# Kernel tuning notes

Measured on AMD Instinct MI355X. Metric: run time of the kernel, lower is better.

The kernel has to match this reference:

```python
import jax, jax.numpy as jnp
import numpy as np

TOP_K = 2

def setup_inputs() -> dict:
    key = jax.random.key(0)
    k1, k2 = jax.random.split(key)
    x = jax.random.normal(k1, (8, 4096, 4096), dtype=jnp.float32)
    # nn.Linear weight [num_experts, dim]
    gate_w = jax.random.normal(k2, (64, 4096), dtype=jnp.float32) * (1.0 / np.sqrt(4096))
    return {"x": x, "gate_w": gate_w}

def reference(x, gate_w):
    # logits: [B, S, E]
    logits = jnp.einsum('bsd,ed->bse', x, gate_w)
    routing_weights = jax.nn.softmax(logits, axis=-1)
    top_weights, top_indices = jax.lax.top_k(routing_weights, TOP_K)
    top_weights = top_weights / jnp.sum(top_weights, axis=-1, keepdims=True)
    return top_weights, top_indices
```

## Files before the change

### kernel.cpp

```cpp
#include <hip/hip_runtime.h>
#include <hip/hip_bf16.h>
#include <math.h>


typedef __attribute__((ext_vector_type(8))) short short8;
typedef __attribute__((ext_vector_type(4))) float f32x4;

#define TPB 32
#define TAU 1e-4f
#define LROW 68

__device__ __forceinline__ void cvt8(const float4* v, short8* hi, short8* lo) {
    const float* f = reinterpret_cast<const float*>(v);
#pragma unroll
    for (int j = 0; j < 8; ++j) {
        __hip_bfloat16 h = __float2bfloat16(f[j]);
        float r = f[j] - __bfloat162float(h);
        __hip_bfloat16 l = __float2bfloat16(r);
        (*hi)[j] = (short)*reinterpret_cast<unsigned short*>(&h);
        (*lo)[j] = (short)*reinterpret_cast<unsigned short*>(&l);
    }
}

__global__ void prep_b(const float* __restrict__ gw,
                       short8* __restrict__ bh, short8* __restrict__ bl) {
    const int tid = blockIdx.x * 256 + threadIdx.x;
    const int ln  = tid & 63;
    const int w   = (tid >> 6) & 127;
    const int nt  = tid >> 13;
    const int row = nt * 16 + (ln & 15);
    const int k   = w * 32 + ((ln >> 4) << 3);
    float4 v[2];
    v[0] = *reinterpret_cast<const float4*>(gw + (long)row * 4096 + k);
    v[1] = *reinterpret_cast<const float4*>(gw + (long)row * 4096 + k + 4);
    short8 h, l;
    cvt8(v, &h, &l);
    bh[tid] = h;
    bl[tid] = l;
}

#define LOADA(BUF, S) do {                                                    \
    (BUF)[0][0] = *reinterpret_cast<const float4*>(pA0 + (S) * 32);           \
    (BUF)[0][1] = *reinterpret_cast<const float4*>(pA0 + (S) * 32 + 4);       \
    (BUF)[1][0] = *reinterpret_cast<const float4*>(pA1 + (S) * 32);           \
    (BUF)[1][1] = *reinterpret_cast<const float4*>(pA1 + (S) * 32 + 4);       \
} while (0)

#define COMPUTE(BUF, BH, BL) do {                                             \
    short8 ah0, al0, ah1, al1;                                                \
    cvt8((BUF)[0], &ah0, &al0);                                               \
    cvt8((BUF)[1], &ah1, &al1);                                               \
    _Pragma("unroll")                                                         \
    for (int nt = 0; nt < 4; ++nt) {                                          \
        acc[0][nt] = __builtin_amdgcn_mfma_f32_16x16x32_bf16(ah0, (BH)[nt], acc[0][nt], 0, 0, 0); \
        acc[0][nt] = __builtin_amdgcn_mfma_f32_16x16x32_bf16(ah0, (BL)[nt], acc[0][nt], 0, 0, 0); \
        acc[0][nt] = __builtin_amdgcn_mfma_f32_16x16x32_bf16(al0, (BH)[nt], acc[0][nt], 0, 0, 0); \
        acc[0][nt] = __builtin_amdgcn_mfma_f32_16x16x32_bf16(al0, (BL)[nt], acc[0][nt], 0, 0, 0); \
        acc[1][nt] = __builtin_amdgcn_mfma_f32_16x16x32_bf16(ah1, (BH)[nt], acc[1][nt], 0, 0, 0); \
        acc[1][nt] = __builtin_amdgcn_mfma_f32_16x16x32_bf16(ah1, (BL)[nt], acc[1][nt], 0, 0, 0); \
        acc[1][nt] = __builtin_amdgcn_mfma_f32_16x16x32_bf16(al1, (BH)[nt], acc[1][nt], 0, 0, 0); \
        acc[1][nt] = __builtin_amdgcn_mfma_f32_16x16x32_bf16(al1, (BL)[nt], acc[1][nt], 0, 0, 0); \
    }                                                                         \
} while (0)

template<bool PACKED>
__global__ __launch_bounds__(256, 4)
void router_mfma_topk(const float* __restrict__ x,
                      const float* __restrict__ gw,
                      const short8* __restrict__ bhp,
                      const short8* __restrict__ blp,
                      float* __restrict__ out,
                      int M, int K) {
    __shared__ float Lp[4 * TPB * LROW];
    __shared__ int flags[TPB];
    __shared__ double Ld4[4][64];

    const int t  = threadIdx.x;
    const int wv = t >> 6;
    const int ln = t & 63;
    const int fr = ln & 15;
    const int q  = ln >> 4;
    const long tok0 = (long)blockIdx.x * TPB;

    const int kbase = wv * 1024 + q * 8;
    const float* pA0 = x + (tok0 + fr) * (long)K + kbase;
    const float* pA1 = x + (tok0 + 16 + fr) * (long)K + kbase;
    const float* pBf[4];
#pragma unroll
    for (int nt = 0; nt < 4; ++nt)
        pBf[nt] = gw + (long)(nt * 16 + fr) * (long)K + kbase;
    const int bidx0 = (wv * 32) * 64 + ln;

    f32x4 acc[2][4];
#pragma unroll
    for (int mt = 0; mt < 2; ++mt)
#pragma unroll
        for (int nt = 0; nt < 4; ++nt) acc[mt][nt] = (f32x4){0.f, 0.f, 0.f, 0.f};

    float4 A0[2][2], A1[2][2];
    LOADA(A0, 0);

    for (int it = 0; it < 16; ++it) {
        const int s0 = 2 * it;
        short8 bh0[4], bl0[4];
        if constexpr (PACKED) {
#pragma unroll
            for (int nt = 0; nt < 4; ++nt) {
                const int idx = bidx0 + nt * 8192 + s0 * 64;
                bh0[nt] = bhp[idx];
                bl0[nt] = blp[idx];
            }
        } else {
#pragma unroll
            for (int nt = 0; nt < 4; ++nt) {
                float4 v[2];
                v[0] = *reinterpret_cast<const float4*>(pBf[nt] + s0 * 32);
                v[1] = *reinterpret_cast<const float4*>(pBf[nt] + s0 * 32 + 4);
                cvt8(v, &bh0[nt], &bl0[nt]);
            }
        }
        LOADA(A1, s0 + 1);
        __builtin_amdgcn_sched_barrier(0);
        COMPUTE(A0, bh0, bl0);

        short8 bh1[4], bl1[4];
        if constexpr (PACKED) {
#pragma unroll
            for (int nt = 0; nt < 4; ++nt) {
                const int idx = bidx0 + nt * 8192 + (s0 + 1) * 64;
                bh1[nt] = bhp[idx];
                bl1[nt] = blp[idx];
            }
        } else {
#pragma unroll
            for (int nt = 0; nt < 4; ++nt) {
                float4 v[2];
                v[0] = *reinterpret_cast<const float4*>(pBf[nt] + (s0 + 1) * 32);
                v[1] = *reinterpret_cast<const float4*>(pBf[nt] + (s0 + 1) * 32 + 4);
                cvt8(v, &bh1[nt], &bl1[nt]);
            }
        }
        if (it < 15) LOADA(A0, s0 + 2);
        __builtin_amdgcn_sched_barrier(0);
        COMPUTE(A1, bh1, bl1);
    }

    float* myLp = Lp + wv * (TPB * LROW);
#pragma unroll
    for (int mt = 0; mt < 2; ++mt)
#pragma unroll
        for (int nt = 0; nt < 4; ++nt)
#pragma unroll
            for (int r = 0; r < 4; ++r) {
                const int tokl = mt * 16 + q * 4 + r;
                const int e    = nt * 16 + fr;
                myLp[tokl * LROW + e] = acc[mt][nt][r];
            }
    __syncthreads();

    for (int i = t; i < TPB * LROW; i += 256)
        Lp[i] = (Lp[i] + Lp[TPB * LROW + i])
              + (Lp[2 * TPB * LROW + i] + Lp[3 * TPB * LROW + i]);
    __syncthreads();

    if (t < TPB) {
        const float* row = Lp + (long)t * LROW;
        float m1 = -INFINITY, m2 = -INFINITY, m3 = -INFINITY;
        int i1 = 0, i2 = 0;
#pragma unroll 8
        for (int e = 0; e < 64; ++e) {
            const float v = row[e];
            if (v > m1)      { m3 = m2; m2 = m1; i2 = i1; m1 = v; i1 = e; }
            else if (v > m2) { m3 = m2; m2 = v; i2 = e; }
            else if (v > m3) { m3 = v; }
        }
        const float e2 = expf(m2 - m1);
        const float s  = 1.0f + e2;

        const long g = tok0 + t;
        out[2 * g + 0] = 1.0f / s;
        out[2 * g + 1] = e2 / s;
        float* oi = out + 2 * (long)M;
        oi[2 * g + 0] = (float)i1;
        oi[2 * g + 1] = (float)i2;

        flags[t] = ((m1 - m2) < TAU) | ((m2 - m3) < TAU);
    }
    __syncthreads();

    for (int tk = 0; tk < TPB; ++tk) {
        if (flags[tk]) {
            const float* xr = x + (tok0 + tk) * (long)K + wv * 1024;
            const float* gr = gw + (long)ln * (long)K + wv * 1024;
            double s0 = 0.0, s1 = 0.0, s2 = 0.0, s3 = 0.0;
            for (int k = 0; k < 1024; k += 4) {
                const float4 a = *reinterpret_cast<const float4*>(xr + k);
                const float4 b = *reinterpret_cast<const float4*>(gr + k);
                s0 = fma((double)a.x, (double)b.x, s0);
                s1 = fma((double)a.y, (double)b.y, s1);
                s2 = fma((double)a.z, (double)b.z, s2);
                s3 = fma((double)a.w, (double)b.w, s3);
            }
            Ld4[wv][ln] = (s0 + s1) + (s2 + s3);
            __syncthreads();
            if (t == 0) {
                double m1 = -INFINITY, m2 = -INFINITY;
                int i1 = 0, i2 = 0;
                for (int e = 0; e < 64; ++e) {
                    const double v = Ld4[0][e] + Ld4[1][e] + Ld4[2][e] + Ld4[3][e];
                    if (v > m1)      { m2 = m1; i2 = i1; m1 = v; i1 = e; }
                    else if (v > m2) { m2 = v; i2 = e; }
                }
                const double e2 = exp(m2 - m1);
                const double s  = 1.0 + e2;
                const long g = tok0 + tk;
                out[2 * g + 0] = (float)(1.0 / s);
                out[2 * g + 1] = (float)(e2 / s);
                float* oi = out + 2 * (long)M;
                oi[2 * g + 0] = (float)i1;
                oi[2 * g + 1] = (float)i2;
            }
            __syncthreads();
        }
    }
}

extern "C" void kernel_launch(void* const* d_in, const int* in_sizes, int n_in,
                              void* d_out, int out_size, void* d_ws, size_t ws_size,
                              hipStream_t stream) {
    const float* x  = (const float*)d_in[0];
    const float* gw = (const float*)d_in[1];
    float* out = (float*)d_out;

    const int K = 4096;
    const int M = in_sizes[0] / K;
    const int nblocks = M / TPB;

    if (ws_size >= (1u << 20)) {
        short8* bh = (short8*)d_ws;
        short8* bl = bh + 32768;
        prep_b<<<128, 256, 0, stream>>>(gw, bh, bl);
        router_mfma_topk<true><<<nblocks, 256, 0, stream>>>(x, gw, bh, bl, out, M, K);
    } else {
        router_mfma_topk<false><<<nblocks, 256, 0, stream>>>(x, gw, nullptr, nullptr, out, M, K);
    }
}
```

Measured before the change: 236.9 us.

## Split waves 2x2 over tokens and K halves in router MFMA kernel

Work is now split across the four waves as two token groups times two K halves, instead of four K quarters each covering all 32 tokens. Each wave keeps four accumulators instead of eight, and the cross-wave LDS reduction sums two partials instead of four. The cost is that each packed weight fragment is reused by only 16 tokens per wave, so weight loads per MFMA double. The unpacked-weight fallback is removed, so the kernel now assumes the workspace is large enough.

Result: slower. 275.9 us (+16.5%).

```diff
diff --git a/kernel.cpp b/kernel.cpp
--- a/kernel.cpp
+++ b/kernel.cpp
@@ -39,128 +39,82 @@
     bl[tid] = l;
 }
 
-#define LOADA(BUF, S) do {                                                    \
-    (BUF)[0][0] = *reinterpret_cast<const float4*>(pA0 + (S) * 32);           \
-    (BUF)[0][1] = *reinterpret_cast<const float4*>(pA0 + (S) * 32 + 4);       \
-    (BUF)[1][0] = *reinterpret_cast<const float4*>(pA1 + (S) * 32);           \
-    (BUF)[1][1] = *reinterpret_cast<const float4*>(pA1 + (S) * 32 + 4);       \
+#define WSTEP(ACUR, APRE, PREOFF, WIDX) do {                                  \
+    const long bi = bidx0 + (long)(WIDX) * 64;                                \
+    short8 bh0 = bhp[bi], bh1 = bhp[bi + 8192],                               \
+           bh2 = bhp[bi + 16384], bh3 = bhp[bi + 24576];                      \
+    short8 bl0 = blp[bi], bl1 = blp[bi + 8192],                               \
+           bl2 = blp[bi + 16384], bl3 = blp[bi + 24576];                      \
+    (APRE)[0] = *reinterpret_cast<const float4*>(pA + (PREOFF));              \
+    (APRE)[1] = *reinterpret_cast<const float4*>(pA + (PREOFF) + 4);          \
+    __builtin_amdgcn_sched_barrier(0);                                        \
+    short8 ah, al;                                                            \
+    cvt8((ACUR), &ah, &al);                                                   \
+    acc[0] = __builtin_amdgcn_mfma_f32_16x16x32_bf16(ah, bh0, acc[0], 0, 0, 0); \
+    acc[0] = __builtin_amdgcn_mfma_f32_16x16x32_bf16(ah, bl0, acc[0], 0, 0, 0); \
+    acc[0] = __builtin_amdgcn_mfma_f32_16x16x32_bf16(al, bh0, acc[0], 0, 0, 0); \
+    acc[0] = __builtin_amdgcn_mfma_f32_16x16x32_bf16(al, bl0, acc[0], 0, 0, 0); \
+    acc[1] = __builtin_amdgcn_mfma_f32_16x16x32_bf16(ah, bh1, acc[1], 0, 0, 0); \
+    acc[1] = __builtin_amdgcn_mfma_f32_16x16x32_bf16(ah, bl1, acc[1], 0, 0, 0); \
+    acc[1] = __builtin_amdgcn_mfma_f32_16x16x32_bf16(al, bh1, acc[1], 0, 0, 0); \
+    acc[1] = __builtin_amdgcn_mfma_f32_16x16x32_bf16(al, bl1, acc[1], 0, 0, 0); \
+    acc[2] = __builtin_amdgcn_mfma_f32_16x16x32_bf16(ah, bh2, acc[2], 0, 0, 0); \
+    acc[2] = __builtin_amdgcn_mfma_f32_16x16x32_bf16(ah, bl2, acc[2], 0, 0, 0); \
+    acc[2] = __builtin_amdgcn_mfma_f32_16x16x32_bf16(al, bh2, acc[2], 0, 0, 0); \
+    acc[2] = __builtin_amdgcn_mfma_f32_16x16x32_bf16(al, bl2, acc[2], 0, 0, 0); \
+    acc[3] = __builtin_amdgcn_mfma_f32_16x16x32_bf16(ah, bh3, acc[3], 0, 0, 0); \
+    acc[3] = __builtin_amdgcn_mfma_f32_16x16x32_bf16(ah, bl3, acc[3], 0, 0, 0); \
+    acc[3] = __builtin_amdgcn_mfma_f32_16x16x32_bf16(al, bh3, acc[3], 0, 0, 0); \
+    acc[3] = __builtin_amdgcn_mfma_f32_16x16x32_bf16(al, bl3, acc[3], 0, 0, 0); \
 } while (0)
 
-#define COMPUTE(BUF, BH, BL) do {                                             \
-    short8 ah0, al0, ah1, al1;                                                \
-    cvt8((BUF)[0], &ah0, &al0);                                               \
-    cvt8((BUF)[1], &ah1, &al1);                                               \
-    _Pragma("unroll")                                                         \
-    for (int nt = 0; nt < 4; ++nt) {                                          \
-        acc[0][nt] = __builtin_amdgcn_mfma_f32_16x16x32_bf16(ah0, (BH)[nt], acc[0][nt], 0, 0, 0); \
-        acc[0][nt] = __builtin_amdgcn_mfma_f32_16x16x32_bf16(ah0, (BL)[nt], acc[0][nt], 0, 0, 0); \
-        acc[0][nt] = __builtin_amdgcn_mfma_f32_16x16x32_bf16(al0, (BH)[nt], acc[0][nt], 0, 0, 0); \
-        acc[0][nt] = __builtin_amdgcn_mfma_f32_16x16x32_bf16(al0, (BL)[nt], acc[0][nt], 0, 0, 0); \
-        acc[1][nt] = __builtin_amdgcn_mfma_f32_16x16x32_bf16(ah1, (BH)[nt], acc[1][nt], 0, 0, 0); \
-        acc[1][nt] = __builtin_amdgcn_mfma_f32_16x16x32_bf16(ah1, (BL)[nt], acc[1][nt], 0, 0, 0); \
-        acc[1][nt] = __builtin_amdgcn_mfma_f32_16x16x32_bf16(al1, (BH)[nt], acc[1][nt], 0, 0, 0); \
-        acc[1][nt] = __builtin_amdgcn_mfma_f32_16x16x32_bf16(al1, (BL)[nt], acc[1][nt], 0, 0, 0); \
-    }                                                                         \
-} while (0)
-
-template<bool PACKED>
 __global__ __launch_bounds__(256, 4)
 void router_mfma_topk(const float* __restrict__ x,
-                      const float* __restrict__ gw,
                       const short8* __restrict__ bhp,
                       const short8* __restrict__ blp,
+                      const float* __restrict__ gw,
                       float* __restrict__ out,
                       int M, int K) {
-    __shared__ float Lp[4 * TPB * LROW];
+    __shared__ float Lp[2 * TPB * LROW];
     __shared__ int flags[TPB];
     __shared__ double Ld4[4][64];
 
     const int t  = threadIdx.x;
     const int wv = t >> 6;
+    const int km = wv & 1;
+    const int mm = wv >> 1;
     const int ln = t & 63;
     const int fr = ln & 15;
     const int q  = ln >> 4;
     const long tok0 = (long)blockIdx.x * TPB;
 
-    const int kbase = wv * 1024 + q * 8;
-    const float* pA0 = x + (tok0 + fr) * (long)K + kbase;
-    const float* pA1 = x + (tok0 + 16 + fr) * (long)K + kbase;
-    const float* pBf[4];
+    const float* pA = x + (tok0 + mm * 16 + fr) * (long)K + km * 2048 + q * 8;
+    const long bidx0 = (long)(km * 64) * 64 + ln;
+
+    f32x4 acc[4];
+#pragma unroll
+    for (int nt = 0; nt < 4; ++nt) acc[nt] = (f32x4){0.f, 0.f, 0.f, 0.f};
+
+    float4 a0[2], a1[2];
+    a0[0] = *reinterpret_cast<const float4*>(pA);
+    a0[1] = *reinterpret_cast<const float4*>(pA + 4);
+
+    for (int i = 0; i < 64; i += 2) {
+        WSTEP(a0, a1, (i + 1) * 32, i);
+        const int pre = (i + 2 < 64) ? (i + 2) * 32 : 0;
+        WSTEP(a1, a0, pre, i + 1);
+    }
+
+    float* myLp = Lp + km * (TPB * LROW);
 #pragma unroll
     for (int nt = 0; nt < 4; ++nt)
-        pBf[nt] = gw + (long)(nt * 16 + fr) * (long)K + kbase;
-    const int bidx0 = (wv * 32) * 64 + ln;
-
-    f32x4 acc[2][4];
 #pragma unroll
-    for (int mt = 0; mt < 2; ++mt)
-#pragma unroll
-        for (int nt = 0; nt < 4; ++nt) acc[mt][nt] = (f32x4){0.f, 0.f, 0.f, 0.f};
-
-    float4 A0[2][2], A1[2][2];
-    LOADA(A0, 0);
-
-    for (int it = 0; it < 16; ++it) {
-        const int s0 = 2 * it;
-        short8 bh0[4], bl0[4];
-        if constexpr (PACKED) {
-#pragma unroll
-            for (int nt = 0; nt < 4; ++nt) {
-                const int idx = bidx0 + nt * 8192 + s0 * 64;
-                bh0[nt] = bhp[idx];
-                bl0[nt] = blp[idx];
-            }
-        } else {
-#pragma unroll
-            for (int nt = 0; nt < 4; ++nt) {
-                float4 v[2];
-                v[0] = *reinterpret_cast<const float4*>(pBf[nt] + s0 * 32);
-                v[1] = *reinterpret_cast<const float4*>(pBf[nt] + s0 * 32 + 4);
-                cvt8(v, &bh0[nt], &bl0[nt]);
-            }
-        }
-        LOADA(A1, s0 + 1);
-        __builtin_amdgcn_sched_barrier(0);
-        COMPUTE(A0, bh0, bl0);
-
-        short8 bh1[4], bl1[4];
-        if constexpr (PACKED) {
-#pragma unroll
-            for (int nt = 0; nt < 4; ++nt) {
-                const int idx = bidx0 + nt * 8192 + (s0 + 1) * 64;
-                bh1[nt] = bhp[idx];
-                bl1[nt] = blp[idx];
-            }
-        } else {
-#pragma unroll
-            for (int nt = 0; nt < 4; ++nt) {
-                float4 v[2];
-                v[0] = *reinterpret_cast<const float4*>(pBf[nt] + (s0 + 1) * 32);
-                v[1] = *reinterpret_cast<const float4*>(pBf[nt] + (s0 + 1) * 32 + 4);
-                cvt8(v, &bh1[nt], &bl1[nt]);
-            }
-        }
-        if (it < 15) LOADA(A0, s0 + 2);
-        __builtin_amdgcn_sched_barrier(0);
-        COMPUTE(A1, bh1, bl1);
-    }
-
-    float* myLp = Lp + wv * (TPB * LROW);
-#pragma unroll
-    for (int mt = 0; mt < 2; ++mt)
-#pragma unroll
-        for (int nt = 0; nt < 4; ++nt)
-#pragma unroll
-            for (int r = 0; r < 4; ++r) {
-                const int tokl = mt * 16 + q * 4 + r;
-                const int e    = nt * 16 + fr;
-                myLp[tokl * LROW + e] = acc[mt][nt][r];
-            }
+        for (int r = 0; r < 4; ++r)
+            myLp[(mm * 16 + q * 4 + r) * LROW + nt * 16 + fr] = acc[nt][r];
     __syncthreads();
 
     for (int i = t; i < TPB * LROW; i += 256)
-        Lp[i] = (Lp[i] + Lp[TPB * LROW + i])
-              + (Lp[2 * TPB * LROW + i] + Lp[3 * TPB * LROW + i]);
+        Lp[i] += Lp[TPB * LROW + i];
     __syncthreads();
 
     if (t < TPB) {
@@ -236,12 +190,8 @@
     const int M = in_sizes[0] / K;
     const int nblocks = M / TPB;
 
-    if (ws_size >= (1u << 20)) {
-        short8* bh = (short8*)d_ws;
-        short8* bl = bh + 32768;
-        prep_b<<<128, 256, 0, stream>>>(gw, bh, bl);
-        router_mfma_topk<true><<<nblocks, 256, 0, stream>>>(x, gw, bh, bl, out, M, K);
-    } else {
-        router_mfma_topk<false><<<nblocks, 256, 0, stream>>>(x, gw, nullptr, nullptr, out, M, K);
-    }
+    short8* bh = (short8*)d_ws;
+    short8* bl = bh + 32768;
+    prep_b<<<128, 256, 0, stream>>>(gw, bh, bl);
+    router_mfma_topk<<<nblocks, 256, 0, stream>>>(x, bh, bl, gw, out, M, K);
 }
```
